# Kernel tuning notes

Measured on AMD Instinct MI355X. Metric: run time of the kernel, lower is better.

## Reference

```python
import jax, jax.numpy as jnp
import numpy as np

N, C, H, W = 64, 64, 8, 8   # batch, channels (img_net_out_dim), feature-map HxW
E = 256                      # ques_rnn_hidden_dim
G = 512                      # rn_g_dim
FD = 512                     # rn_f_dim
GIN = 2 * (C + 2) + E        # g-MLP input dim = 388
NUM_CLASSES = 2


def _lin(key, din, dout):
    # kaiming-uniform-like init for a Linear stored as (in, out)
    bound = float(np.sqrt(6.0 / din))
    w = jax.random.uniform(key, (din, dout), minval=-bound, maxval=bound, dtype=jnp.float32)
    b = jnp.zeros((dout,), dtype=jnp.float32)
    return w, b


def setup_inputs() -> dict:
    key = jax.random.key(0)
    ks = jax.random.split(key, 9)
    img = jax.random.normal(ks[0], (N, C, H, W), dtype=jnp.float32)
    ques = jax.random.normal(ks[1], (N, E), dtype=jnp.float32)
    g_w1, g_b1 = _lin(ks[2], GIN, G)
    g_w2, g_b2 = _lin(ks[3], G, G)
    g_w3, g_b3 = _lin(ks[4], G, G)
    g_w4, g_b4 = _lin(ks[5], G, G)
    f_w1, f_b1 = _lin(ks[6], G, FD)
    f_w2, f_b2 = _lin(ks[7], FD, FD)
    f_w3, f_b3 = _lin(ks[8], FD, NUM_CLASSES)
    return dict(img=img, ques=ques,
                g_w1=g_w1, g_b1=g_b1, g_w2=g_w2, g_b2=g_b2,
                g_w3=g_w3, g_b3=g_b3, g_w4=g_w4, g_b4=g_b4,
                f_w1=f_w1, f_b1=f_b1, f_w2=f_w2, f_b2=f_b2,
                f_w3=f_w3, f_b3=f_b3)


def _img_to_pairs(img, ques):
    # img: (n, c, h, w), ques: (n, e) -> pairs: (n, hw*hw, 2*(c+2)+e)
    n, c, h, w = img.shape
    hw = h * w
    cells = img.reshape(n, c, hw)
    idx = jnp.arange(hw)
    loc = jnp.stack([idx // w, idx % w], axis=0).astype(img.dtype)  # (2, hw)
    cells = jnp.concatenate([cells, jnp.broadcast_to(loc[None], (n, 2, hw))], axis=1)
    feats = cells.transpose(0, 2, 1)  # (n, hw, c+2)
    fdim = feats.shape[-1]
    one = jnp.broadcast_to(feats[:, :, None, :], (n, hw, hw, fdim))   # object i
    two = jnp.broadcast_to(feats[:, None, :, :], (n, hw, hw, fdim))   # object j
    q = jnp.broadcast_to(ques[:, None, None, :], (n, hw, hw, ques.shape[-1]))
    return jnp.concatenate([one, two, q], axis=-1).reshape(n, hw * hw, -1)


def reference(img, ques, g_w1, g_b1, g_w2, g_b2, g_w3, g_b3, g_w4, g_b4,
              f_w1, f_b1, f_w2, f_b2, f_w3, f_b3):
    pairs = _img_to_pairs(img, ques)                      # (N, HW^2, GIN)
    hdd = jax.nn.relu(pairs @ g_w1 + g_b1)                # shared g-MLP over all pairs
    hdd = jax.nn.relu(hdd @ g_w2 + g_b2)
    hdd = jax.nn.relu(hdd @ g_w3 + g_b3)
    hdd = jax.nn.relu(hdd @ g_w4 + g_b4)
    context = hdd.mean(axis=1)                            # (N, G)
    z = jax.nn.relu(context @ f_w1 + f_b1)                # f-MLP (dropout = identity in eval)
    z = jax.nn.relu(z @ f_w2 + f_b2)
    scores = z @ f_w3 + f_b3                              # (N, 2)
    return jax.nn.log_softmax(scores, axis=1)
```

## Files before the change

kernel.cpp:

```cpp
#include <hip/hip_runtime.h>

typedef unsigned short u16;
typedef unsigned int u32;
typedef _Float16 f16;

using half8 = __attribute__((ext_vector_type(8))) _Float16;
using f32x4 = __attribute__((ext_vector_type(4))) float;
using f32x16 = __attribute__((ext_vector_type(16))) float;


__global__ __launch_bounds__(512) void prep_p12(const float* __restrict__ img,
                                                const float* __restrict__ gw1,
                                                float* __restrict__ P1,
                                                f16* __restrict__ P2c) {
    const int blk = blockIdx.x;
    const int n = blk >> 3;
    const int c0 = (blk & 7) * 8;
    const int t = threadIdx.x;
    __shared__ float feats[8][68];
    for (int idx = t; idx < 8 * 66; idx += 512) {
        int rr = idx / 66, cc = idx % 66, cell = c0 + rr;
        float v;
        if (cc < 64)       v = img[((size_t)(n * 64 + cc)) * 64 + cell];
        else if (cc == 64) v = (float)(cell >> 3);
        else               v = (float)(cell & 7);
        feats[rr][cc] = v;
    }
    __syncthreads();
    const int g = t;
    float a1[8], a2[8];
#pragma unroll
    for (int r = 0; r < 8; ++r) { a1[r] = 0.f; a2[r] = 0.f; }
    for (int c = 0; c < 66; ++c) {
        float wa = gw1[(size_t)c * 512 + g];
        float wb = gw1[(size_t)(66 + c) * 512 + g];
#pragma unroll
        for (int r = 0; r < 8; ++r) {
            a1[r] += feats[r][c] * wa;
            a2[r] += feats[r][c] * wb;
        }
    }
    const size_t cb = (size_t)n * 32768 + (g >> 4) * 1024 + ((g >> 3) & 1) * 512 + (g & 7);
#pragma unroll
    for (int r = 0; r < 8; ++r) {
        P1[((size_t)(n * 64 + c0 + r)) * 512 + g] = a1[r];
        P2c[cb + (c0 + r) * 8] = (f16)a2[r];
    }
}

__global__ __launch_bounds__(512) void prep_q2(const float* __restrict__ ques,
                                               const float* __restrict__ gw1,
                                               const float* __restrict__ gb1,
                                               const float* __restrict__ P1,
                                               f16* __restrict__ P1c,
                                               float* __restrict__ Ctx) {
    const int n = blockIdx.x;
    const int t = threadIdx.x;
    __shared__ float q[256];
    if (t < 256) q[t] = ques[(size_t)n * 256 + t];
    __syncthreads();
    float acc = gb1[t];
    for (int e = 0; e < 256; ++e)
        acc += q[e] * gw1[(size_t)(132 + e) * 512 + t];
    const float* src = P1 + (((size_t)(n * 64)) << 9) + t;
    const size_t cb = (size_t)n * 32768 + (t >> 4) * 1024 + ((t >> 3) & 1) * 512 + (t & 7);
    for (int r = 0; r < 64; ++r)
        P1c[cb + r * 8] = (f16)(src[(size_t)r * 512] + acc);
    Ctx[(size_t)n * 512 + t] = 0.f;
}

__global__ void transpose_w(const float* __restrict__ W2, const float* __restrict__ W3,
                            const float* __restrict__ W4, f16* __restrict__ T2,
                            f16* __restrict__ T3, f16* __restrict__ T4) {
    const int L = blockIdx.z;
    const float* W = (L == 0) ? W2 : ((L == 1) ? W3 : W4);
    f16* T = (L == 0) ? T2 : ((L == 1) ? T3 : T4);
    __shared__ float tile[32][33];
    const int bx = blockIdx.x * 32;
    const int by = blockIdx.y * 32;
    const int tx = threadIdx.x, ty = threadIdx.y;
    for (int r = ty; r < 32; r += 8)
        tile[r][tx] = W[(size_t)(by + r) * 512 + bx + tx];
    __syncthreads();
    for (int r = ty; r < 32; r += 8) {
        const int n = bx + r, k = by + tx;
        T[(size_t)(k >> 4) * 8192 + ((k >> 3) & 1) * 4096 + n * 8 + (k & 7)] =
            (f16)tile[tx][r];
    }
}

__global__ __launch_bounds__(512, 4) void fused_g234(
    const f16* __restrict__ P1c, const f16* __restrict__ P2c,
    const f16* __restrict__ T2, const f16* __restrict__ T3,
    const f16* __restrict__ T4, const float* __restrict__ gb2,
    const float* __restrict__ gb3, const float* __restrict__ gb4,
    float* __restrict__ Ctx) {
    const int tid = threadIdx.x;
    const int lane = tid & 63;
    const int lane31 = lane & 31;
    const int khalf = lane >> 5;
    const int wv = tid >> 6;
    const int b = blockIdx.x;
    const int nb = b >> 6;
    const int i0 = b & 63;

    __shared__ alignas(16) f16 H[32 * 1024];

    const f16* P1b = P1c + (size_t)nb * 32768;
    const f16* P2b = P2c + (size_t)nb * 32768;

#pragma unroll
    for (int u = 0; u < 4; ++u) {
        const int ks = wv * 4 + u;
        const int cb = ks * 1024 + khalf * 512;
        const int f = ((ks & 1) << 1) | khalf;
        half8 x = *(const half8*)(P1b + cb + i0 * 8);
#pragma unroll
        for (int rr = 0; rr < 2; ++rr) {
            half8 y = *(const half8*)(P2b + cb + (rr * 32 + lane31) * 8);
            half8 s = x + y;
            s = __builtin_elementwise_max(s, (half8)(f16)0.f);
            *(half8*)&H[cb + (rr * 32 + (lane31 ^ f)) * 8] = s;
        }
    }
    __syncthreads();

    f32x16 acc[2][2];
#pragma unroll
    for (int mi = 0; mi < 2; ++mi)
#pragma unroll
        for (int ni = 0; ni < 2; ++ni)
#pragma unroll
            for (int r = 0; r < 16; ++r)
                acc[mi][ni][r] = 0.f;

    const int aoffE = khalf * 512 + (lane31 ^ khalf) * 8;
    const int aoffO = khalf * 512 + (lane31 ^ (2 | khalf)) * 8;
    const u32 boff = (u32)(khalf * 4096 + (wv * 64 + lane31) * 8) * 2u;

    auto mfma4 = [&](half8 a0, half8 a1, half8 b0, half8 b1) {
        __builtin_amdgcn_s_setprio(1);
        acc[0][0] = __builtin_amdgcn_mfma_f32_32x32x16_f16(a0, b0, acc[0][0], 0, 0, 0);
        acc[0][1] = __builtin_amdgcn_mfma_f32_32x32x16_f16(a0, b1, acc[0][1], 0, 0, 0);
        acc[1][0] = __builtin_amdgcn_mfma_f32_32x32x16_f16(a1, b0, acc[1][0], 0, 0, 0);
        acc[1][1] = __builtin_amdgcn_mfma_f32_32x32x16_f16(a1, b1, acc[1][1], 0, 0, 0);
        __builtin_amdgcn_s_setprio(0);
    };

    auto run_layer = [&](const f16* __restrict__ T) {
        const char* Tb = (const char*)T;
        u32 vo = boff;
        half8 bA0 = *(const half8*)(Tb + vo);
        half8 bA1 = *(const half8*)(Tb + vo + 512);
        half8 bB0, bB1;
#pragma unroll 1
        for (int k2 = 0; k2 < 16; ++k2) {
            const int e0 = aoffE + k2 * 2048;
            vo += 16384;
            bB0 = *(const half8*)(Tb + vo);
            bB1 = *(const half8*)(Tb + vo + 512);
            {
                half8 a0 = *(const half8*)&H[e0];
                half8 a1 = *(const half8*)&H[e0 + 256];
                mfma4(a0, a1, bA0, bA1);
            }
            if (k2 < 15) {
                vo += 16384;
                bA0 = *(const half8*)(Tb + vo);
                bA1 = *(const half8*)(Tb + vo + 512);
            }
            {
                const int o0 = aoffO + k2 * 2048 + 1024;
                half8 a0 = *(const half8*)&H[o0];
                half8 a1 = *(const half8*)&H[o0 + 256];
                mfma4(a0, a1, bB0, bB1);
            }
        }
    };

    auto writeback = [&](const float* __restrict__ bias) {
        float bb[2];
#pragma unroll
        for (int ni = 0; ni < 2; ++ni)
            bb[ni] = bias[wv * 64 + ni * 32 + lane31];
        __syncthreads();
#pragma unroll
        for (int ni = 0; ni < 2; ++ni) {
            const int c = wv * 64 + ni * 32 + lane31;
            const int cbase = (c >> 4) * 1024 + ((c >> 3) & 1) * 512;
            const int fw = (((c >> 4) & 1) << 1) | ((c >> 3) & 1);
            const int j = c & 7;
#pragma unroll
            for (int mi = 0; mi < 2; ++mi) {
#pragma unroll
                for (int r = 0; r < 16; ++r) {
                    const int row = mi * 32 + (r & 3) + 4 * khalf + 8 * (r >> 2);
                    float v = fmaxf(acc[mi][ni][r] + bb[ni], 0.f);
                    H[cbase + (row ^ fw) * 8 + j] = (f16)v;
                    acc[mi][ni][r] = 0.f;
                }
            }
        }
        __syncthreads();
    };

    run_layer(T2);
    writeback(gb2);
    run_layer(T3);
    writeback(gb3);
    run_layer(T4);

#pragma unroll
    for (int ni = 0; ni < 2; ++ni) {
        const int col = wv * 64 + ni * 32 + lane31;
        float bb = gb4[col];
        float s = 0.f;
#pragma unroll
        for (int mi = 0; mi < 2; ++mi)
#pragma unroll
            for (int r = 0; r < 16; ++r)
                s += fmaxf(acc[mi][ni][r] + bb, 0.f);
        s += __shfl_xor(s, 32, 64);
        if (khalf == 0)
            atomicAdd(&Ctx[(((size_t)nb) << 9) + col], s);
    }
}

__global__ __launch_bounds__(512) void fmlp_layer(
    const float* __restrict__ In, const float* __restrict__ Wt,
    const float* __restrict__ bias, float* __restrict__ Out, float scale) {
    const int n = blockIdx.x, cs = blockIdx.y;
    const int t = threadIdx.x;
    const int col = cs * 64 + (t & 63);
    const int seg = t >> 6;
    __shared__ float a[512];
    __shared__ float red[512];
    a[t] = In[(size_t)n * 512 + t] * scale;
    __syncthreads();
    float p = 0.f;
#pragma unroll 8
    for (int i = seg * 64; i < seg * 64 + 64; ++i)
        p += a[i] * Wt[(size_t)i * 512 + col];
    red[t] = p;
    __syncthreads();
    if (t < 64) {
        float v = bias[col];
#pragma unroll
        for (int sg = 0; sg < 8; ++sg) v += red[sg * 64 + t];
        Out[(size_t)n * 512 + cs * 64 + t] = fmaxf(v, 0.f);
    }
}

__global__ __launch_bounds__(64) void fmlp_out(
    const float* __restrict__ A2, const float* __restrict__ fw3,
    const float* __restrict__ fb3, float* __restrict__ out) {
    const int n = blockIdx.x;
    const int lane = threadIdx.x;
    float s0 = 0.f, s1 = 0.f;
    for (int i = lane; i < 512; i += 64) {
        float v = A2[(size_t)n * 512 + i];
        s0 += v * fw3[i * 2];
        s1 += v * fw3[i * 2 + 1];
    }
#pragma unroll
    for (int d = 1; d < 64; d <<= 1) {
        s0 += __shfl_xor(s0, d, 64);
        s1 += __shfl_xor(s1, d, 64);
    }
    if (lane == 0) {
        s0 += fb3[0];
        s1 += fb3[1];
        float m = fmaxf(s0, s1);
        float l = logf(expf(s0 - m) + expf(s1 - m)) + m;
        out[n * 2 + 0] = s0 - l;
        out[n * 2 + 1] = s1 - l;
    }
}

extern "C" void kernel_launch(void* const* d_in, const int* in_sizes, int n_in,
                              void* d_out, int out_size, void* d_ws, size_t ws_size,
                              hipStream_t stream) {
    const float* img  = (const float*)d_in[0];
    const float* ques = (const float*)d_in[1];
    const float* gw1  = (const float*)d_in[2];
    const float* gb1  = (const float*)d_in[3];
    const float* gw2  = (const float*)d_in[4];
    const float* gb2  = (const float*)d_in[5];
    const float* gw3  = (const float*)d_in[6];
    const float* gb3  = (const float*)d_in[7];
    const float* gw4  = (const float*)d_in[8];
    const float* gb4  = (const float*)d_in[9];
    const float* fw1  = (const float*)d_in[10];
    const float* fb1  = (const float*)d_in[11];
    const float* fw2  = (const float*)d_in[12];
    const float* fb2  = (const float*)d_in[13];
    const float* fw3  = (const float*)d_in[14];
    const float* fb3  = (const float*)d_in[15];

    char* ws = (char*)d_ws;
    size_t off = 0;
    float* P1  = (float*)(ws + off); off += (size_t)4096 * 512 * 4;
    f16* P1c = (f16*)(ws + off); off += (size_t)4096 * 512 * 2;
    f16* P2c = (f16*)(ws + off); off += (size_t)4096 * 512 * 2;
    float* Ctx = (float*)(ws + off); off += (size_t)64 * 512 * 4;
    float* Z1  = (float*)(ws + off); off += (size_t)64 * 512 * 4;
    float* Z2  = (float*)(ws + off); off += (size_t)64 * 512 * 4;
    f16* T2 = (f16*)(ws + off); off += (size_t)512 * 512 * 2;
    f16* T3 = (f16*)(ws + off); off += (size_t)512 * 512 * 2;
    f16* T4 = (f16*)(ws + off); off += (size_t)512 * 512 * 2;

    prep_p12<<<512, 512, 0, stream>>>(img, gw1, P1, P2c);
    prep_q2<<<64, 512, 0, stream>>>(ques, gw1, gb1, P1, P1c, Ctx);
    transpose_w<<<dim3(16, 16, 3), dim3(32, 8), 0, stream>>>(gw2, gw3, gw4, T2, T3, T4);

    fused_g234<<<4096, 512, 0, stream>>>(P1c, P2c, T2, T3, T4, gb2, gb3, gb4, Ctx);

    fmlp_layer<<<dim3(64, 8), 512, 0, stream>>>(Ctx, fw1, fb1, Z1, 1.0f / 4096.0f);
    fmlp_layer<<<dim3(64, 8), 512, 0, stream>>>(Z1, fw2, fb2, Z2, 1.0f);
    fmlp_out<<<64, 64, 0, stream>>>(Z2, fw3, fb3, (float*)d_out);
}
```

Measured before the change: 491.2 us.

## Fuse layer-1 pair build into first GEMM and merge f-MLP kernels

The question-projection term is now computed before prep_p12, which adds it in directly and writes P1c as fp16. This removes the fp32 P1 buffer and its round trip. In the main kernel the layer-1 relu(x+y) tile is no longer staged into shared memory. It is built on the fly from global P1c/P2c inside the first GEMM's k-loop, which drops a shared-memory pass and a barrier but adds redundant global loads per k-step. The three f-MLP launches are merged into one kernel per batch row, cutting launch count at the cost of less parallelism (64 blocks, serial 512-length dot products).

After: 580.2 us. +18.1%, slower.

```diff
diff --git a/kernel.cpp b/kernel.cpp
--- a/kernel.cpp
+++ b/kernel.cpp
@@ -9,9 +9,27 @@
 using f32x16 = __attribute__((ext_vector_type(16))) float;
 
 
+__global__ __launch_bounds__(512) void prep_qc(const float* __restrict__ ques,
+                                               const float* __restrict__ gw1,
+                                               const float* __restrict__ gb1,
+                                               float* __restrict__ Qc,
+                                               float* __restrict__ Ctx) {
+    const int n = blockIdx.x;
+    const int t = threadIdx.x;
+    __shared__ float q[256];
+    if (t < 256) q[t] = ques[(size_t)n * 256 + t];
+    __syncthreads();
+    float acc = gb1[t];
+    for (int e = 0; e < 256; ++e)
+        acc += q[e] * gw1[(size_t)(132 + e) * 512 + t];
+    Qc[(size_t)n * 512 + t] = acc;
+    Ctx[(size_t)n * 512 + t] = 0.f;
+}
+
 __global__ __launch_bounds__(512) void prep_p12(const float* __restrict__ img,
                                                 const float* __restrict__ gw1,
-                                                float* __restrict__ P1,
+                                                const float* __restrict__ Qc,
+                                                f16* __restrict__ P1c,
                                                 f16* __restrict__ P2c) {
     const int blk = blockIdx.x;
     const int n = blk >> 3;
@@ -40,33 +58,13 @@
             a2[r] += feats[r][c] * wb;
         }
     }
+    const float qc = Qc[(size_t)n * 512 + g];
     const size_t cb = (size_t)n * 32768 + (g >> 4) * 1024 + ((g >> 3) & 1) * 512 + (g & 7);
 #pragma unroll
     for (int r = 0; r < 8; ++r) {
-        P1[((size_t)(n * 64 + c0 + r)) * 512 + g] = a1[r];
+        P1c[cb + (c0 + r) * 8] = (f16)(a1[r] + qc);
         P2c[cb + (c0 + r) * 8] = (f16)a2[r];
     }
-}
-
-__global__ __launch_bounds__(512) void prep_q2(const float* __restrict__ ques,
-                                               const float* __restrict__ gw1,
-                                               const float* __restrict__ gb1,
-                                               const float* __restrict__ P1,
-                                               f16* __restrict__ P1c,
-                                               float* __restrict__ Ctx) {
-    const int n = blockIdx.x;
-    const int t = threadIdx.x;
-    __shared__ float q[256];
-    if (t < 256) q[t] = ques[(size_t)n * 256 + t];
-    __syncthreads();
-    float acc = gb1[t];
-    for (int e = 0; e < 256; ++e)
-        acc += q[e] * gw1[(size_t)(132 + e) * 512 + t];
-    const float* src = P1 + (((size_t)(n * 64)) << 9) + t;
-    const size_t cb = (size_t)n * 32768 + (t >> 4) * 1024 + ((t >> 3) & 1) * 512 + (t & 7);
-    for (int r = 0; r < 64; ++r)
-        P1c[cb + r * 8] = (f16)(src[(size_t)r * 512] + acc);
-    Ctx[(size_t)n * 512 + t] = 0.f;
 }
 
 __global__ void transpose_w(const float* __restrict__ W2, const float* __restrict__ W3,
@@ -109,22 +107,6 @@
     const f16* P1b = P1c + (size_t)nb * 32768;
     const f16* P2b = P2c + (size_t)nb * 32768;
 
-#pragma unroll
-    for (int u = 0; u < 4; ++u) {
-        const int ks = wv * 4 + u;
-        const int cb = ks * 1024 + khalf * 512;
-        const int f = ((ks & 1) << 1) | khalf;
-        half8 x = *(const half8*)(P1b + cb + i0 * 8);
-#pragma unroll
-        for (int rr = 0; rr < 2; ++rr) {
-            half8 y = *(const half8*)(P2b + cb + (rr * 32 + lane31) * 8);
-            half8 s = x + y;
-            s = __builtin_elementwise_max(s, (half8)(f16)0.f);
-            *(half8*)&H[cb + (rr * 32 + (lane31 ^ f)) * 8] = s;
-        }
-    }
-    __syncthreads();
-
     f32x16 acc[2][2];
 #pragma unroll
     for (int mi = 0; mi < 2; ++mi)
@@ -136,6 +118,9 @@
 
     const int aoffE = khalf * 512 + (lane31 ^ khalf) * 8;
     const int aoffO = khalf * 512 + (lane31 ^ (2 | khalf)) * 8;
+    const int ybase0 = khalf * 512 + lane31 * 8;
+    const int ybase1 = khalf * 512 + (32 + lane31) * 8;
+    const int xbase  = khalf * 512 + i0 * 8;
     const u32 boff = (u32)(khalf * 4096 + (wv * 64 + lane31) * 8) * 2u;
 
     auto mfma4 = [&](half8 a0, half8 a1, half8 b0, half8 b1) {
@@ -145,6 +130,42 @@
         acc[1][0] = __builtin_amdgcn_mfma_f32_32x32x16_f16(a1, b0, acc[1][0], 0, 0, 0);
         acc[1][1] = __builtin_amdgcn_mfma_f32_32x32x16_f16(a1, b1, acc[1][1], 0, 0, 0);
         __builtin_amdgcn_s_setprio(0);
+    };
+
+    auto run_layer2 = [&](const f16* __restrict__ T) {
+        const char* Tb = (const char*)T;
+        u32 vo = boff;
+        half8 bA0 = *(const half8*)(Tb + vo);
+        half8 bA1 = *(const half8*)(Tb + vo + 512);
+        half8 bB0, bB1;
+#pragma unroll 1
+        for (int k2 = 0; k2 < 16; ++k2) {
+            const int cb = k2 * 2048;
+            vo += 16384;
+            bB0 = *(const half8*)(Tb + vo);
+            bB1 = *(const half8*)(Tb + vo + 512);
+            {
+                half8 x  = *(const half8*)(P1b + cb + xbase);
+                half8 y0 = *(const half8*)(P2b + cb + ybase0);
+                half8 y1 = *(const half8*)(P2b + cb + ybase1);
+                half8 a0 = __builtin_elementwise_max(x + y0, (half8)(f16)0.f);
+                half8 a1 = __builtin_elementwise_max(x + y1, (half8)(f16)0.f);
+                mfma4(a0, a1, bA0, bA1);
+            }
+            if (k2 < 15) {
+                vo += 16384;
+                bA0 = *(const half8*)(Tb + vo);
+                bA1 = *(const half8*)(Tb + vo + 512);
+            }
+            {
+                half8 x  = *(const half8*)(P1b + cb + 1024 + xbase);
+                half8 y0 = *(const half8*)(P2b + cb + 1024 + ybase0);
+                half8 y1 = *(const half8*)(P2b + cb + 1024 + ybase1);
+                half8 a0 = __builtin_elementwise_max(x + y0, (half8)(f16)0.f);
+                half8 a1 = __builtin_elementwise_max(x + y1, (half8)(f16)0.f);
+                mfma4(a0, a1, bB0, bB1);
+            }
+        }
     };
 
     auto run_layer = [&](const f16* __restrict__ T) {
@@ -178,12 +199,12 @@
         }
     };
 
-    auto writeback = [&](const float* __restrict__ bias) {
+    auto writeback = [&](const float* __restrict__ bias, bool lead_barrier) {
         float bb[2];
 #pragma unroll
         for (int ni = 0; ni < 2; ++ni)
             bb[ni] = bias[wv * 64 + ni * 32 + lane31];
-        __syncthreads();
+        if (lead_barrier) __syncthreads();
 #pragma unroll
         for (int ni = 0; ni < 2; ++ni) {
             const int c = wv * 64 + ni * 32 + lane31;
@@ -204,10 +225,10 @@
         __syncthreads();
     };
 
-    run_layer(T2);
-    writeback(gb2);
+    run_layer2(T2);
+    writeback(gb2, false);
     run_layer(T3);
-    writeback(gb3);
+    writeback(gb3, true);
     run_layer(T4);
 
 #pragma unroll
@@ -226,50 +247,45 @@
     }
 }
 
-__global__ __launch_bounds__(512) void fmlp_layer(
-    const float* __restrict__ In, const float* __restrict__ Wt,
-    const float* __restrict__ bias, float* __restrict__ Out, float scale) {
-    const int n = blockIdx.x, cs = blockIdx.y;
+__global__ __launch_bounds__(512) void fmlp_all(
+    const float* __restrict__ Ctx,
+    const float* __restrict__ fw1, const float* __restrict__ fb1,
+    const float* __restrict__ fw2, const float* __restrict__ fb2,
+    const float* __restrict__ fw3, const float* __restrict__ fb3,
+    float* __restrict__ out) {
+    const int n = blockIdx.x;
     const int t = threadIdx.x;
-    const int col = cs * 64 + (t & 63);
-    const int seg = t >> 6;
+    const int lane = t & 63;
+    const int wvv = t >> 6;
     __shared__ float a[512];
-    __shared__ float red[512];
-    a[t] = In[(size_t)n * 512 + t] * scale;
-    __syncthreads();
-    float p = 0.f;
+    __shared__ float z[512];
+    __shared__ float r0[8], r1[8];
+    a[t] = Ctx[(size_t)n * 512 + t] * (1.0f / 4096.0f);
+    __syncthreads();
+    float p = fb1[t];
 #pragma unroll 8
-    for (int i = seg * 64; i < seg * 64 + 64; ++i)
-        p += a[i] * Wt[(size_t)i * 512 + col];
-    red[t] = p;
-    __syncthreads();
-    if (t < 64) {
-        float v = bias[col];
-#pragma unroll
-        for (int sg = 0; sg < 8; ++sg) v += red[sg * 64 + t];
-        Out[(size_t)n * 512 + cs * 64 + t] = fmaxf(v, 0.f);
-    }
-}
-
-__global__ __launch_bounds__(64) void fmlp_out(
-    const float* __restrict__ A2, const float* __restrict__ fw3,
-    const float* __restrict__ fb3, float* __restrict__ out) {
-    const int n = blockIdx.x;
-    const int lane = threadIdx.x;
-    float s0 = 0.f, s1 = 0.f;
-    for (int i = lane; i < 512; i += 64) {
-        float v = A2[(size_t)n * 512 + i];
-        s0 += v * fw3[i * 2];
-        s1 += v * fw3[i * 2 + 1];
-    }
+    for (int i = 0; i < 512; ++i)
+        p += a[i] * fw1[(size_t)i * 512 + t];
+    z[t] = fmaxf(p, 0.f);
+    __syncthreads();
+    p = fb2[t];
+#pragma unroll 8
+    for (int i = 0; i < 512; ++i)
+        p += z[i] * fw2[(size_t)i * 512 + t];
+    float z2 = fmaxf(p, 0.f);
+    float v0 = z2 * fw3[t * 2];
+    float v1 = z2 * fw3[t * 2 + 1];
 #pragma unroll
     for (int d = 1; d < 64; d <<= 1) {
-        s0 += __shfl_xor(s0, d, 64);
-        s1 += __shfl_xor(s1, d, 64);
-    }
-    if (lane == 0) {
-        s0 += fb3[0];
-        s1 += fb3[1];
+        v0 += __shfl_xor(v0, d, 64);
+        v1 += __shfl_xor(v1, d, 64);
+    }
+    if (lane == 0) { r0[wvv] = v0; r1[wvv] = v1; }
+    __syncthreads();
+    if (t == 0) {
+        float s0 = fb3[0], s1 = fb3[1];
+#pragma unroll
+        for (int w = 0; w < 8; ++w) { s0 += r0[w]; s1 += r1[w]; }
         float m = fmaxf(s0, s1);
         float l = logf(expf(s0 - m) + expf(s1 - m)) + m;
         out[n * 2 + 0] = s0 - l;
@@ -299,23 +315,19 @@
 
     char* ws = (char*)d_ws;
     size_t off = 0;
-    float* P1  = (float*)(ws + off); off += (size_t)4096 * 512 * 4;
     f16* P1c = (f16*)(ws + off); off += (size_t)4096 * 512 * 2;
     f16* P2c = (f16*)(ws + off); off += (size_t)4096 * 512 * 2;
+    float* Qc  = (float*)(ws + off); off += (size_t)64 * 512 * 4;
     float* Ctx = (float*)(ws + off); off += (size_t)64 * 512 * 4;
-    float* Z1  = (float*)(ws + off); off += (size_t)64 * 512 * 4;
-    float* Z2  = (float*)(ws + off); off += (size_t)64 * 512 * 4;
     f16* T2 = (f16*)(ws + off); off += (size_t)512 * 512 * 2;
     f16* T3 = (f16*)(ws + off); off += (size_t)512 * 512 * 2;
     f16* T4 = (f16*)(ws + off); off += (size_t)512 * 512 * 2;
 
-    prep_p12<<<512, 512, 0, stream>>>(img, gw1, P1, P2c);
-    prep_q2<<<64, 512, 0, stream>>>(ques, gw1, gb1, P1, P1c, Ctx);
+    prep_qc<<<64, 512, 0, stream>>>(ques, gw1, gb1, Qc, Ctx);
+    prep_p12<<<512, 512, 0, stream>>>(img, gw1, Qc, P1c, P2c);
     transpose_w<<<dim3(16, 16, 3), dim3(32, 8), 0, stream>>>(gw2, gw3, gw4, T2, T3, T4);
 
     fused_g234<<<4096, 512, 0, stream>>>(P1c, P2c, T2, T3, T4, gb2, gb3, gb4, Ctx);
 
-    fmlp_layer<<<dim3(64, 8), 512, 0, stream>>>(Ctx, fw1, fb1, Z1, 1.0f / 4096.0f);
-    fmlp_layer<<<dim3(64, 8), 512, 0, stream>>>(Z1, fw2, fb2, Z2, 1.0f);
-    fmlp_out<<<64, 64, 0, stream>>>(Z2, fw3, fb3, (float*)d_out);
-}
+    fmlp_all<<<64, 512, 0, stream>>>(Ctx, fw1, fb1, fw2, fb2, fw3, fb3, (float*)d_out);
+}
```
